# Optimization experiments

Hardware: AMD Instinct MI355X
Metric: run time of the kernel (lower is better)

## Reference

```python
import jax, jax.numpy as jnp
import numpy as np

B, T, S, H, NUM_HEAD = 4, 1024, 1024, 1024, 16
CAUSAL = True
EPS = 1e-5            # torch nn.LayerNorm default
NEG = -float(2 ** 32)  # masked_fill value in the source


def setup_inputs() -> dict:
    key = jax.random.key(0)
    ks = jax.random.split(key, 8)
    queries = jax.random.normal(ks[0], (B, T, H), jnp.float32)
    keys = jax.random.normal(ks[1], (B, S, H), jnp.float32)
    queries_mask = jax.random.randint(ks[2], (B, T, 1), 0, 2).astype(jnp.int32)
    keys_mask = jax.random.randint(ks[3], (B, S, 1), 0, 2).astype(jnp.int32)
    Wq = jax.random.normal(ks[4], (H, H), jnp.float32) * 0.02
    Wk = jax.random.normal(ks[5], (H, H), jnp.float32) * 0.02
    Wv = jax.random.normal(ks[6], (H, H), jnp.float32) * 0.02
    bq = jnp.zeros((H,), jnp.float32)
    bk = jnp.zeros((H,), jnp.float32)
    bv = jnp.zeros((H,), jnp.float32)
    gamma = jnp.ones((H,), jnp.float32)
    beta = jnp.zeros((H,), jnp.float32)
    return {"queries": queries, "queries_mask": queries_mask, "keys": keys,
            "keys_mask": keys_mask, "Wq": Wq, "bq": bq, "Wk": Wk, "bk": bk,
            "Wv": Wv, "bv": bv, "gamma": gamma, "beta": beta}


def _layernorm(x, gamma, beta):
    m = jnp.mean(x, axis=-1, keepdims=True)
    v = jnp.mean((x - m) ** 2, axis=-1, keepdims=True)  # biased var, as torch
    return gamma * (x - m) / jnp.sqrt(v + EPS) + beta


def reference(queries, queries_mask, keys, keys_mask, Wq, bq, Wk, bk, Wv, bv, gamma, beta):
    dh = H // NUM_HEAD
    # ReLU-activated QKV projections (torch Linear: x @ W.T + b)
    Q = jax.nn.relu(queries @ Wq.T + bq)            # (B,T,H)
    K = jax.nn.relu(keys @ Wk.T + bk)               # (B,S,H)
    V = jax.nn.relu(keys @ Wv.T + bv)               # (B,S,H)
    # chunk along feature dim then cat along batch == (h, B, L, dh) layout
    Qh = Q.reshape(B, T, NUM_HEAD, dh).transpose(2, 0, 1, 3)
    Kh = K.reshape(B, S, NUM_HEAD, dh).transpose(2, 0, 1, 3)
    Vh = V.reshape(B, S, NUM_HEAD, dh).transpose(2, 0, 1, 3)
    # scaled by sqrt(hidden_size), NOT sqrt(head_dim) — faithful to source
    scores = jnp.einsum('hbtd,hbsd->hbts', Qh, Kh) / float(np.sqrt(H))
    # padding mask via outer product of the two masks
    qm = queries_mask[..., 0].astype(jnp.float32)   # (B,T)
    km = keys_mask[..., 0].astype(jnp.float32)      # (B,S)
    pad = (qm[:, :, None] * km[:, None, :]) == 0.0  # (B,T,S) True -> masked
    scores = jnp.where(pad[None], NEG, scores)
    if CAUSAL:
        tri = jnp.triu(jnp.ones((T, S), bool), k=1)  # triu(ones)-eye == strict upper
        scores = jnp.where(tri[None, None], NEG, scores)
    attn = jax.nn.softmax(scores, axis=-1)
    out = jnp.einsum('hbts,hbsd->hbtd', attn, Vh)   # (h,B,T,dh)
    out = out.transpose(1, 2, 0, 3).reshape(B, T, H)  # cat heads back on feature dim
    out = out * queries_mask.astype(jnp.float32)
    return _layernorm(out + queries, gamma, beta)
```

## Files before the change

### kernel.cpp

```cpp
#include <hip/hip_runtime.h>
#include <hip/hip_bf16.h>
#include <math.h>

#define B_ 4
#define T_ 1024
#define S_ 1024
#define H_ 1024
#define NH_ 16
#define DH_ 64
#define NEGV -4294967296.0f
#define EPS_ 1e-5f

typedef __attribute__((ext_vector_type(8))) short short8;
typedef __attribute__((ext_vector_type(8))) unsigned short ushort8;
typedef __attribute__((ext_vector_type(4))) unsigned short ushort4v;
typedef __attribute__((ext_vector_type(4))) unsigned int uint4v;
typedef __attribute__((ext_vector_type(4))) float f32x4;

__device__ __forceinline__ unsigned short f2bf(float x) {
    unsigned int u = __float_as_uint(x);
    u += 0x7FFF + ((u >> 16) & 1);
    return (unsigned short)(u >> 16);
}

__device__ __forceinline__ float bf2f(unsigned short u) {
    return __uint_as_float(((unsigned int)u) << 16);
}

__device__ __forceinline__ unsigned int pack_bf16(float a, float b) {
    union { __hip_bfloat162 h; unsigned int u; } cv;
    cv.h = __float22bfloat162_rn(float2{a, b});
    return cv.u;
}

__device__ __forceinline__ void gload16(const unsigned short* g, unsigned short* l) {
    __builtin_amdgcn_global_load_lds(
        (const __attribute__((address_space(1))) unsigned int*)g,
        (__attribute__((address_space(3))) unsigned int*)l,
        16, 0, 0);
}

#define VMCNT(n) asm volatile("s_waitcnt vmcnt(" #n ")" ::: "memory")
#define LGKM0()  { asm volatile("s_waitcnt lgkmcnt(0)" ::: "memory"); \
                   __builtin_amdgcn_sched_barrier(0); }

__global__ __launch_bounds__(256) void cast_bf16(
    const float* __restrict__ q, const float* __restrict__ k,
    const float* __restrict__ wq, const float* __restrict__ wk,
    const float* __restrict__ wv,
    unsigned short* __restrict__ dq, unsigned short* __restrict__ dk,
    unsigned short* __restrict__ dwq, unsigned short* __restrict__ dwk,
    unsigned short* __restrict__ dwv)
{
    const int seg = blockIdx.y;
    const float* src; unsigned short* dst; int n;
    switch (seg) {
        case 0:  src = q;  dst = dq;  n = B_*T_*H_; break;
        case 1:  src = k;  dst = dk;  n = B_*S_*H_; break;
        case 2:  src = wq; dst = dwq; n = H_*H_;    break;
        case 3:  src = wk; dst = dwk; n = H_*H_;    break;
        default: src = wv; dst = dwv; n = H_*H_;    break;
    }
    const int i = (blockIdx.x * 256 + threadIdx.x) * 8;
    if (i >= n) return;
    float4 a = *(const float4*)&src[i];
    float4 b = *(const float4*)&src[i + 4];
    ushort8 o;
    o[0] = f2bf(a.x); o[1] = f2bf(a.y); o[2] = f2bf(a.z); o[3] = f2bf(a.w);
    o[4] = f2bf(b.x); o[5] = f2bf(b.y); o[6] = f2bf(b.z); o[7] = f2bf(b.w);
    *(ushort8*)&dst[i] = o;
}

__global__ __launch_bounds__(512, 4) void qkv_mfma(
    const unsigned short* __restrict__ Xq, const unsigned short* __restrict__ Xk,
    const unsigned short* __restrict__ Wq, const unsigned short* __restrict__ Wk,
    const unsigned short* __restrict__ Wv,
    const float* __restrict__ bq, const float* __restrict__ bk,
    const float* __restrict__ bv,
    unsigned short* __restrict__ Qo, unsigned short* __restrict__ Ko,
    unsigned short* __restrict__ Vo)
{
    const int bi = (blockIdx.x & 7) * 96 + (blockIdx.x >> 3);
    const int col_t = bi >> 5, row_t = bi & 31;
    const int which = col_t >> 3;
    const int colW = (col_t & 7) * 128;
    const int row0 = row_t * 128;

    const unsigned short* X = (which == 0) ? Xq : Xk;
    const unsigned short* Wm = (which == 0) ? Wq : (which == 1) ? Wk : Wv;
    const float* bias        = (which == 0) ? bq : (which == 1) ? bk : bv;
    unsigned short* Out      = (which == 0) ? Qo : (which == 1) ? Ko : Vo;

    __shared__ __align__(16) unsigned short S[32768];

    const int tid = threadIdx.x;
    const int wid = tid >> 6, lane = tid & 63, lo = lane & 15, hi = lane >> 4;
    const int wm = wid >> 2, wn = wid & 3;
    const int swr = (lo & 7) << 3;
    const int csw = ((tid & 7) << 3) ^ (((tid >> 3) & 7) << 3);

    auto stageA = [&](int kt) {
        const int k0 = kt << 6;
        unsigned short* dst = &S[(kt & 1) * 16384 + wid * 512];
        #pragma unroll
        for (int u = 0; u < 2; ++u) {
            const int rowT = row0 + u * 64 + (tid >> 3);
            gload16(&X[(size_t)rowT * H_ + k0 + csw], dst + u * 4096);
        }
    };
    auto stageB = [&](int kt) {
        const int k0 = kt << 6;
        unsigned short* dst = &S[(kt & 1) * 16384 + 8192 + wid * 512];
        #pragma unroll
        for (int u = 0; u < 2; ++u) {
            const int n = u * 64 + (tid >> 3);
            gload16(&Wm[(size_t)(colW + n) * H_ + k0 + csw], dst + u * 4096);
        }
    };

    short8 afr[4][2], bfr[2][2];
    f32x4 acc[4][2] = {};

    auto readA = [&](int boff) {
        #pragma unroll
        for (int i2 = 0; i2 < 4; ++i2)
            #pragma unroll
            for (int kc = 0; kc < 2; ++kc)
                afr[i2][kc] = *(const short8*)
                    &S[boff + (wm*64 + i2*16 + lo)*64 + ((kc*32 + hi*8) ^ swr)];
    };
    auto readB = [&](int boff) {
        #pragma unroll
        for (int j2 = 0; j2 < 2; ++j2)
            #pragma unroll
            for (int kc = 0; kc < 2; ++kc)
                bfr[j2][kc] = *(const short8*)
                    &S[boff + 8192 + (wn*32 + j2*16 + lo)*64 + ((kc*32 + hi*8) ^ swr)];
    };

    float bj[2];
    #pragma unroll
    for (int j2 = 0; j2 < 2; ++j2)
        bj[j2] = bias[colW + wn*32 + j2*16 + lo];

    stageA(0); stageB(0); stageA(1); stageB(1);
    VMCNT(4);
    __builtin_amdgcn_s_barrier();

    for (int it = 0; it < 16; ++it) {
        const int boff = (it & 1) * 16384;
        readA(boff);
        readB(boff);
        LGKM0();
        __builtin_amdgcn_s_barrier();
        if (it <= 13) { stageA(it + 2); stageB(it + 2); }
        __builtin_amdgcn_s_setprio(1);
        #pragma unroll
        for (int i2 = 0; i2 < 4; ++i2)
            #pragma unroll
            for (int j2 = 0; j2 < 2; ++j2)
                #pragma unroll
                for (int kc = 0; kc < 2; ++kc)
                    acc[i2][j2] = __builtin_amdgcn_mfma_f32_16x16x32_bf16(
                        afr[i2][kc], bfr[j2][kc], acc[i2][j2], 0, 0, 0);
        __builtin_amdgcn_s_setprio(0);
        if (it < 14) { VMCNT(4); } else { VMCNT(0); }
        __builtin_amdgcn_s_barrier();
    }

    #pragma unroll
    for (int i2 = 0; i2 < 4; ++i2) {
        const int er = wm*64 + i2*16 + hi*4;
        #pragma unroll
        for (int j2 = 0; j2 < 2; ++j2) {
            const int ec = wn*32 + j2*16 + lo;
            #pragma unroll
            for (int r = 0; r < 4; ++r)
                S[(er + r) * 136 + ec] = f2bf(fmaxf(acc[i2][j2][r] + bj[j2], 0.f));
        }
    }
    __syncthreads();
    #pragma unroll
    for (int u = 0; u < 4; ++u) {
        const int cid = u * 512 + tid;
        const int rr = cid >> 4, ch = cid & 15;
        ushort8 v = *(const ushort8*)&S[rr * 136 + ch * 8];
        *(ushort8*)&Out[(size_t)(row0 + rr) * H_ + colW + ch * 8] = v;
    }
}

__global__ __launch_bounds__(256) void vmean_prep(
    const unsigned short* __restrict__ V, const int* __restrict__ kmask,
    float* __restrict__ vmean_part, int* __restrict__ sfirst)
{
    const int bh = blockIdx.x >> 2, chunk = blockIdx.x & 3;
    const int b = bh >> 4, h = bh & 15;
    const int tid = threadIdx.x;
    const int d8 = tid & 7, sg = tid >> 3;

    __shared__ float red[32][68];
    __shared__ int sf_sh;
    if (tid == 0) sf_sh = S_;

    float acc[8] = {0,0,0,0,0,0,0,0};
    #pragma unroll
    for (int it = 0; it < 8; ++it) {
        const int s = chunk * 256 + sg + it * 32;
        ushort8 v = *(const ushort8*)&V[((size_t)b*S_ + s) * H_ + h*DH_ + d8*8];
        #pragma unroll
        for (int i = 0; i < 8; ++i) acc[i] += bf2f(v[i]);
    }
    #pragma unroll
    for (int i = 0; i < 8; ++i) red[sg][d8*8 + i] = acc[i];

    if (blockIdx.x < B_) {
        int lf = S_;
        #pragma unroll
        for (int u = 0; u < 4; ++u) {
            const int s = tid + u * 256;
            if (kmask[blockIdx.x * S_ + s] != 0) lf = min(lf, s);
        }
        atomicMin(&sf_sh, lf);
    }
    __syncthreads();

    for (int str = 16; str >= 1; str >>= 1) {
        if (sg < str) {
            #pragma unroll
            for (int i = 0; i < 8; ++i)
                red[sg][d8*8 + i] += red[sg + str][d8*8 + i];
        }
        __syncthreads();
    }
    if (tid < 64) vmean_part[blockIdx.x * 64 + tid] = red[0][tid] * (1.f / 1024.f);
    if (blockIdx.x < B_ && tid == 0) sfirst[blockIdx.x] = sf_sh;
}

__global__ __launch_bounds__(256) void attn_mfma(
    const unsigned short* __restrict__ Q, const unsigned short* __restrict__ K,
    const unsigned short* __restrict__ V, const int* __restrict__ kmask,
    const float* __restrict__ vmean_part, const int* __restrict__ sfirst,
    unsigned short* __restrict__ Ob)
{
    const int flat = blockIdx.x;
    const int nf = (flat & 7) * 64 + (flat >> 3);
    const int z = nf & 7, bh = nf >> 3;
    const int b = bh >> 4, h = bh & 15;

    const int tid = threadIdx.x;
    const int wid = tid >> 6, lane = tid & 63, hi = lane >> 4, lo = lane & 15;

    __shared__ unsigned short Ks[2][64][64];
    __shared__ unsigned short Vt[2][64][64];

    const int s_first = sfirst[b];

    const int srow = tid >> 2, d0k = (tid & 3) << 4, swk = (srow & 7) << 3;
    const int sp = tid & 31, dg = tid >> 5;
    const int s2 = sp * 2;
    const int ps = (s2 & 35) | ((s2 & 16) >> 2) | ((s2 & 12) << 1);

    ushort8 krA0, krA1, vrA0, vrA1; int kmA;
    ushort8 krB0, krB1, vrB0, vrB1; int kmB;

    auto stage_load = [&](int s0_, ushort8& k0, ushort8& k1,
                          ushort8& v0, ushort8& v1, int& kmr) {
        const unsigned short* kp = &K[((size_t)b*S_ + s0_ + srow) * H_ + h*DH_ + d0k];
        k0 = *(const ushort8*)kp;
        k1 = *(const ushort8*)(kp + 8);
        const unsigned short* vp = &V[((size_t)b*S_ + s0_ + s2) * H_ + h*DH_ + dg*8];
        v0 = *(const ushort8*)vp;
        v1 = *(const ushort8*)(vp + H_);
        kmr = kmask[b*S_ + s0_ + lane];
    };
    auto stage_write = [&](int pb, const ushort8& k0, const ushort8& k1,
                           const ushort8& v0, const ushort8& v1) {
        *(ushort8*)&Ks[pb][srow][d0k ^ swk]       = k0;
        *(ushort8*)&Ks[pb][srow][(d0k + 8) ^ swk] = k1;
        #pragma unroll
        for (int i = 0; i < 8; ++i) {
            const int d = dg*8 + i;
            const unsigned int pk = (unsigned int)(unsigned short)v0[i]
                                  | ((unsigned int)(unsigned short)v1[i] << 16);
            *(unsigned int*)&Vt[pb][d][ps ^ ((d & 7) << 3)] = pk;
        }
    };

    for (int item = 0; item < 2; ++item) {
        const int qt = item ? z : (15 - z);
        const int t0 = qt * 64;
        const int ntiles = qt + 1;
        const int tq = t0 + wid*16 + lo;

        short8 qf0, qf1;
        {
            const unsigned short* qp =
                &Q[((size_t)b*T_ + t0 + wid*16 + lo) * H_ + h*DH_ + hi*8];
            qf0 = *(const short8*)qp;
            qf1 = *(const short8*)(qp + 32);
        }

        float m = -INFINITY, l = 0.f;
        f32x4 oacc[4] = {{0,0,0,0},{0,0,0,0},{0,0,0,0},{0,0,0,0}};

        auto compute = [&](int pb, int s0, int kmr) {
            const unsigned long long kmb = __ballot(kmr != 0);
            f32x4 sc[4] = {{0,0,0,0},{0,0,0,0},{0,0,0,0},{0,0,0,0}};
            const int swq = (lo & 7) << 3;
            __builtin_amdgcn_s_setprio(1);
            #pragma unroll
            for (int n = 0; n < 4; ++n) {
                short8 kfa = *(const short8*)&Ks[pb][n*16 + lo][(hi*8) ^ swq];
                sc[n] = __builtin_amdgcn_mfma_f32_16x16x32_bf16(kfa, qf0, sc[n], 0, 0, 0);
                short8 kfb = *(const short8*)&Ks[pb][n*16 + lo][(32 + hi*8) ^ swq];
                sc[n] = __builtin_amdgcn_mfma_f32_16x16x32_bf16(kfb, qf1, sc[n], 0, 0, 0);
            }
            __builtin_amdgcn_s_setprio(0);
            float p[4][4];
            float rm = -INFINITY;
            #pragma unroll
            for (int n = 0; n < 4; ++n)
                #pragma unroll
                for (int r = 0; r < 4; ++r) {
                    const int sl = n*16 + hi*4 + r;
                    const bool msk = !((kmb >> sl) & 1ull) || (s0 + sl > tq);
                    const float v = sc[n][r] * 0.03125f;
                    p[n][r] = msk ? NEGV : v;
                    rm = fmaxf(rm, p[n][r]);
                }
            rm = fmaxf(rm, __shfl_xor(rm, 16));
            rm = fmaxf(rm, __shfl_xor(rm, 32));
            if (__any(rm > m + 8.f)) {
                const float mn  = fmaxf(m, rm);
                const float scl = __expf(m - mn);
                m = mn;
                l *= scl;
                #pragma unroll
                for (int r = 0; r < 4; ++r) {
                    const float os = __shfl(scl, hi*4 + r);
                    oacc[0][r] *= os; oacc[1][r] *= os;
                    oacc[2][r] *= os; oacc[3][r] *= os;
                }
            }
            float ts = 0.f;
            #pragma unroll
            for (int n = 0; n < 4; ++n)
                #pragma unroll
                for (int r = 0; r < 4; ++r) {
                    p[n][r] = __expf(p[n][r] - m);
                    ts += p[n][r];
                }
            ts += __shfl_xor(ts, 16);
            ts += __shfl_xor(ts, 32);
            l += ts;
            unsigned int pk0[4], pk1[4];
            #pragma unroll
            for (int n = 0; n < 4; ++n) {
                pk0[n] = pack_bf16(p[n][0], p[n][1]);
                pk1[n] = pack_bf16(p[n][2], p[n][3]);
            }
            __builtin_amdgcn_s_setprio(1);
            #pragma unroll
            for (int cch = 0; cch < 2; ++cch) {
                uint4v u;
                u.x = pk0[2*cch];   u.y = pk1[2*cch];
                u.z = pk0[2*cch+1]; u.w = pk1[2*cch+1];
                const short8 pf = __builtin_bit_cast(short8, u);
                #pragma unroll
                for (int n2 = 0; n2 < 4; ++n2) {
                    const int d = n2*16 + lo;
                    const short8 vf =
                        *(const short8*)&Vt[pb][d][(cch*32 + hi*8) ^ ((d & 7) << 3)];
                    oacc[n2] = __builtin_amdgcn_mfma_f32_16x16x32_bf16(pf, vf, oacc[n2], 0, 0, 0);
                }
            }
            __builtin_amdgcn_s_setprio(0);
        };

        __syncthreads();
        stage_load(0, krA0, krA1, vrA0, vrA1, kmA);
        int t = 0;
        for (;;) {
            stage_write(0, krA0, krA1, vrA0, vrA1);
            if (t + 1 < ntiles) stage_load((t+1) << 6, krB0, krB1, vrB0, vrB1, kmB);
            __syncthreads();
            compute(0, t << 6, kmA);
            if (++t >= ntiles) break;

            stage_write(1, krB0, krB1, vrB0, vrB1);
            if (t + 1 < ntiles) stage_load((t+1) << 6, krA0, krA1, vrA0, vrA1, kmA);
            __syncthreads();
            compute(1, t << 6, kmB);
            if (++t >= ntiles) break;
        }

        const float inv = 1.0f / l;
        #pragma unroll
        for (int r = 0; r < 4; ++r) {
            const float ir = __shfl(inv, hi*4 + r);
            const int trow = t0 + wid*16 + hi*4 + r;
            unsigned short* dst = &Ob[((size_t)b*T_ + trow) * H_ + h*DH_ + lo];
            if (trow < s_first) {
                #pragma unroll
                for (int g = 0; g < 4; ++g) {
                    float vm = vmean_part[(bh*4 + 0)*64 + lo + g*16]
                             + vmean_part[(bh*4 + 1)*64 + lo + g*16]
                             + vmean_part[(bh*4 + 2)*64 + lo + g*16]
                             + vmean_part[(bh*4 + 3)*64 + lo + g*16];
                    dst[g*16] = f2bf(vm);
                }
            } else {
                dst[0]  = f2bf(oacc[0][r] * ir);
                dst[16] = f2bf(oacc[1][r] * ir);
                dst[32] = f2bf(oacc[2][r] * ir);
                dst[48] = f2bf(oacc[3][r] * ir);
            }
        }
    }
}

__global__ __launch_bounds__(256) void ln_kernel(
    const unsigned short* __restrict__ Ob, float* __restrict__ Out,
    const float* __restrict__ queries, const int* __restrict__ qmask,
    const float* __restrict__ gamma, const float* __restrict__ beta)
{
    const int row = blockIdx.x;
    const int tid = threadIdx.x;
    const float qm = (float)qmask[row];

    ushort4v a4 = *(const ushort4v*)&Ob[(size_t)row * H_ + tid*4];
    float4 q4 = *(const float4*)&queries[(size_t)row * H_ + tid*4];
    float x0 = bf2f(a4.x) * qm + q4.x;
    float x1 = bf2f(a4.y) * qm + q4.y;
    float x2 = bf2f(a4.z) * qm + q4.z;
    float x3 = bf2f(a4.w) * qm + q4.w;

    float sum = x0 + x1 + x2 + x3;
    float sq  = x0*x0 + x1*x1 + x2*x2 + x3*x3;
    #pragma unroll
    for (int off = 32; off >= 1; off >>= 1) {
        sum += __shfl_down(sum, off);
        sq  += __shfl_down(sq,  off);
    }
    __shared__ float rs[4], rq[4];
    const int wid = tid >> 6, lane = tid & 63;
    if (lane == 0) { rs[wid] = sum; rq[wid] = sq; }
    __syncthreads();
    const float tot  = rs[0] + rs[1] + rs[2] + rs[3];
    const float totq = rq[0] + rq[1] + rq[2] + rq[3];
    const float mean = tot * (1.f / H_);
    const float var  = totq * (1.f / H_) - mean * mean;
    const float rstd = rsqrtf(var + EPS_);

    float4 g4 = *(const float4*)&gamma[tid*4];
    float4 b4 = *(const float4*)&beta[tid*4];
    float4 y;
    y.x = (x0 - mean) * rstd * g4.x + b4.x;
    y.y = (x1 - mean) * rstd * g4.y + b4.y;
    y.z = (x2 - mean) * rstd * g4.z + b4.z;
    y.w = (x3 - mean) * rstd * g4.w + b4.w;
    *(float4*)&Out[(size_t)row * H_ + tid*4] = y;
}

extern "C" void kernel_launch(void* const* d_in, const int* in_sizes, int n_in,
                              void* d_out, int out_size, void* d_ws, size_t ws_size,
                              hipStream_t stream)
{
    const float* queries = (const float*)d_in[0];
    const int*   qmask   = (const int*)  d_in[1];
    const float* keys    = (const float*)d_in[2];
    const int*   kmask   = (const int*)  d_in[3];
    const float* Wq      = (const float*)d_in[4];
    const float* bq      = (const float*)d_in[5];
    const float* Wk      = (const float*)d_in[6];
    const float* bk      = (const float*)d_in[7];
    const float* Wv      = (const float*)d_in[8];
    const float* bv      = (const float*)d_in[9];
    const float* gamma   = (const float*)d_in[10];
    const float* beta    = (const float*)d_in[11];
    float* out = (float*)d_out;

    unsigned short* Xqb = (unsigned short*)d_ws;
    unsigned short* Xkb = Xqb + (size_t)B_*T_*H_;
    unsigned short* Wqb = Xkb + (size_t)B_*S_*H_;
    unsigned short* Wkb = Wqb + (size_t)H_*H_;
    unsigned short* Wvb = Wkb + (size_t)H_*H_;
    unsigned short* Qb  = Wvb + (size_t)H_*H_;
    unsigned short* Kb  = Qb  + (size_t)B_*T_*H_;
    unsigned short* Vb  = Kb  + (size_t)B_*S_*H_;
    float* vmeanF = (float*)Xqb;
    int*   sfirstI = (int*)(vmeanF + 256*64);
    unsigned short* Ob = Xkb;

    dim3 gc((B_*T_*H_/8 + 255)/256, 5, 1);
    cast_bf16<<<gc, 256, 0, stream>>>(queries, keys, Wq, Wk, Wv,
                                      Xqb, Xkb, Wqb, Wkb, Wvb);

    qkv_mfma<<<768, 512, 0, stream>>>(Xqb, Xkb, Wqb, Wkb, Wvb,
                                      bq, bk, bv, Qb, Kb, Vb);

    vmean_prep<<<256, 256, 0, stream>>>(Vb, kmask, vmeanF, sfirstI);

    attn_mfma<<<512, 256, 0, stream>>>(Qb, Kb, Vb, kmask, vmeanF, sfirstI, Ob);

    ln_kernel<<<B_*T_, 256, 0, stream>>>(Ob, out, queries, qmask, gamma, beta);
}
```

Before: 92.32 us.

## Fuse fp32-to-bf16 activation cast into QKV GEMM A-tile staging

Removes the separate cast pass over queries and keys. The QKV GEMM now loads fp32 activations into registers, converts them to bf16 and writes them to LDS, and a register double buffer keeps the global loads one tile ahead. This saves one write and one read of the bf16 activation copies, but the GEMM reads twice as many activation bytes. It also replaces the async global-to-LDS path for A with register staging, adding VALU conversion work and a full vmcnt(0) wait inside each iteration.

```diff
diff --git a/kernel.cpp b/kernel.cpp
--- a/kernel.cpp
+++ b/kernel.cpp
@@ -45,24 +45,19 @@
                    __builtin_amdgcn_sched_barrier(0); }
 
 __global__ __launch_bounds__(256) void cast_bf16(
-    const float* __restrict__ q, const float* __restrict__ k,
     const float* __restrict__ wq, const float* __restrict__ wk,
     const float* __restrict__ wv,
-    unsigned short* __restrict__ dq, unsigned short* __restrict__ dk,
     unsigned short* __restrict__ dwq, unsigned short* __restrict__ dwk,
     unsigned short* __restrict__ dwv)
 {
     const int seg = blockIdx.y;
-    const float* src; unsigned short* dst; int n;
+    const float* src; unsigned short* dst;
     switch (seg) {
-        case 0:  src = q;  dst = dq;  n = B_*T_*H_; break;
-        case 1:  src = k;  dst = dk;  n = B_*S_*H_; break;
-        case 2:  src = wq; dst = dwq; n = H_*H_;    break;
-        case 3:  src = wk; dst = dwk; n = H_*H_;    break;
-        default: src = wv; dst = dwv; n = H_*H_;    break;
+        case 0:  src = wq; dst = dwq; break;
+        case 1:  src = wk; dst = dwk; break;
+        default: src = wv; dst = dwv; break;
     }
     const int i = (blockIdx.x * 256 + threadIdx.x) * 8;
-    if (i >= n) return;
     float4 a = *(const float4*)&src[i];
     float4 b = *(const float4*)&src[i + 4];
     ushort8 o;
@@ -72,7 +67,7 @@
 }
 
 __global__ __launch_bounds__(512, 4) void qkv_mfma(
-    const unsigned short* __restrict__ Xq, const unsigned short* __restrict__ Xk,
+    const float* __restrict__ Xqf, const float* __restrict__ Xkf,
     const unsigned short* __restrict__ Wq, const unsigned short* __restrict__ Wk,
     const unsigned short* __restrict__ Wv,
     const float* __restrict__ bq, const float* __restrict__ bk,
@@ -86,7 +81,7 @@
     const int colW = (col_t & 7) * 128;
     const int row0 = row_t * 128;
 
-    const unsigned short* X = (which == 0) ? Xq : Xk;
+    const float* Xf = (which == 0) ? Xqf : Xkf;
     const unsigned short* Wm = (which == 0) ? Wq : (which == 1) ? Wk : Wv;
     const float* bias        = (which == 0) ? bq : (which == 1) ? bk : bv;
     unsigned short* Out      = (which == 0) ? Qo : (which == 1) ? Ko : Vo;
@@ -99,13 +94,28 @@
     const int swr = (lo & 7) << 3;
     const int csw = ((tid & 7) << 3) ^ (((tid >> 3) & 7) << 3);
 
-    auto stageA = [&](int kt) {
+    float4 rA[2][4];
+    auto loadA = [&](int kt) {
         const int k0 = kt << 6;
-        unsigned short* dst = &S[(kt & 1) * 16384 + wid * 512];
+        float4* r = rA[kt & 1];
         #pragma unroll
         for (int u = 0; u < 2; ++u) {
             const int rowT = row0 + u * 64 + (tid >> 3);
-            gload16(&X[(size_t)rowT * H_ + k0 + csw], dst + u * 4096);
+            const float* src = &Xf[(size_t)rowT * H_ + k0 + csw];
+            r[u*2]   = *(const float4*)src;
+            r[u*2+1] = *(const float4*)(src + 4);
+        }
+    };
+    auto writeA = [&](int kt) {
+        const float4* r = rA[kt & 1];
+        #pragma unroll
+        for (int u = 0; u < 2; ++u) {
+            ushort8 o;
+            o[0] = f2bf(r[u*2].x);   o[1] = f2bf(r[u*2].y);
+            o[2] = f2bf(r[u*2].z);   o[3] = f2bf(r[u*2].w);
+            o[4] = f2bf(r[u*2+1].x); o[5] = f2bf(r[u*2+1].y);
+            o[6] = f2bf(r[u*2+1].z); o[7] = f2bf(r[u*2+1].w);
+            *(ushort8*)&S[(kt & 1) * 16384 + wid * 512 + u * 4096 + lane * 8] = o;
         }
     };
     auto stageB = [&](int kt) {
@@ -143,8 +153,14 @@
     for (int j2 = 0; j2 < 2; ++j2)
         bj[j2] = bias[colW + wn*32 + j2*16 + lo];
 
-    stageA(0); stageB(0); stageA(1); stageB(1);
+    loadA(0); loadA(1); stageB(0); stageB(1);
+    VMCNT(8);
+    writeA(0);
     VMCNT(4);
+    writeA(1);
+    loadA(2);
+    VMCNT(4);
+    LGKM0();
     __builtin_amdgcn_s_barrier();
 
     for (int it = 0; it < 16; ++it) {
@@ -153,7 +169,14 @@
         readB(boff);
         LGKM0();
         __builtin_amdgcn_s_barrier();
-        if (it <= 13) { stageA(it + 2); stageB(it + 2); }
+        if (it <= 13) {
+            VMCNT(0);
+            writeA(it + 2);
+            stageB(it + 2);
+            if (it <= 12) loadA(it + 3);
+        } else if (it == 14) {
+            VMCNT(0);
+        }
         __builtin_amdgcn_s_setprio(1);
         #pragma unroll
         for (int i2 = 0; i2 < 4; ++i2)
@@ -164,7 +187,6 @@
                     acc[i2][j2] = __builtin_amdgcn_mfma_f32_16x16x32_bf16(
                         afr[i2][kc], bfr[j2][kc], acc[i2][j2], 0, 0, 0);
         __builtin_amdgcn_s_setprio(0);
-        if (it < 14) { VMCNT(4); } else { VMCNT(0); }
         __builtin_amdgcn_s_barrier();
     }
 
@@ -492,11 +514,10 @@
     int*   sfirstI = (int*)(vmeanF + 256*64);
     unsigned short* Ob = Xkb;
 
-    dim3 gc((B_*T_*H_/8 + 255)/256, 5, 1);
-    cast_bf16<<<gc, 256, 0, stream>>>(queries, keys, Wq, Wk, Wv,
-                                      Xqb, Xkb, Wqb, Wkb, Wvb);
-
-    qkv_mfma<<<768, 512, 0, stream>>>(Xqb, Xkb, Wqb, Wkb, Wvb,
+    dim3 gc(H_*H_/8/256, 3, 1);
+    cast_bf16<<<gc, 256, 0, stream>>>(Wq, Wk, Wv, Wqb, Wkb, Wvb);
+
+    qkv_mfma<<<768, 512, 0, stream>>>(queries, keys, Wqb, Wkb, Wvb,
                                       bq, bk, bv, Qb, Kb, Vb);
 
     vmean_prep<<<256, 256, 0, stream>>>(Vb, kmask, vmeanF, sfirstI);
```

New measurement: 218.4 us. 2.37x slower.

## Share K/V tile loads between paired causal query tiles in one pass

Applied to the files above, without the earlier changes.

Instead of processing the high and low query tiles sequentially, each reloading K/V from global memory, the block now streams K/V once and computes both query tiles against each staged tile while the low tile is still within its causal range. This removes the duplicate K/V loads and staging for the low tile and one pass of loop and sync overhead. In exchange it keeps two sets of accumulators and Q fragments live, which raises register pressure and may lower occupancy.

```diff
diff --git a/kernel.cpp b/kernel.cpp
--- a/kernel.cpp
+++ b/kernel.cpp
@@ -286,119 +286,133 @@
         }
     };
 
-    for (int item = 0; item < 2; ++item) {
-        const int qt = item ? z : (15 - z);
-        const int t0 = qt * 64;
-        const int ntiles = qt + 1;
-        const int tq = t0 + wid*16 + lo;
-
-        short8 qf0, qf1;
+    const int qtH = 15 - z, qtL = z;
+    const int t0H = qtH * 64, t0L = qtL * 64;
+    const int ntiles = qtH + 1;
+    const int tqH = t0H + wid*16 + lo;
+    const int tqL = t0L + wid*16 + lo;
+
+    short8 qfH0, qfH1, qfL0, qfL1;
+    {
+        const unsigned short* qp =
+            &Q[((size_t)b*T_ + t0H + wid*16 + lo) * H_ + h*DH_ + hi*8];
+        qfH0 = *(const short8*)qp;
+        qfH1 = *(const short8*)(qp + 32);
+        const unsigned short* qp2 =
+            &Q[((size_t)b*T_ + t0L + wid*16 + lo) * H_ + h*DH_ + hi*8];
+        qfL0 = *(const short8*)qp2;
+        qfL1 = *(const short8*)(qp2 + 32);
+    }
+
+    float mH = -INFINITY, lH = 0.f, mL = -INFINITY, lL = 0.f;
+    f32x4 oH[4] = {{0,0,0,0},{0,0,0,0},{0,0,0,0},{0,0,0,0}};
+    f32x4 oL[4] = {{0,0,0,0},{0,0,0,0},{0,0,0,0},{0,0,0,0}};
+
+    auto compute = [&](int pb, int s0, unsigned long long kmb,
+                       float& m, float& l, f32x4 (&oacc)[4], int tq,
+                       const short8& qf0, const short8& qf1) {
+        f32x4 sc[4] = {{0,0,0,0},{0,0,0,0},{0,0,0,0},{0,0,0,0}};
+        const int swq = (lo & 7) << 3;
+        __builtin_amdgcn_s_setprio(1);
+        #pragma unroll
+        for (int n = 0; n < 4; ++n) {
+            short8 kfa = *(const short8*)&Ks[pb][n*16 + lo][(hi*8) ^ swq];
+            sc[n] = __builtin_amdgcn_mfma_f32_16x16x32_bf16(kfa, qf0, sc[n], 0, 0, 0);
+            short8 kfb = *(const short8*)&Ks[pb][n*16 + lo][(32 + hi*8) ^ swq];
+            sc[n] = __builtin_amdgcn_mfma_f32_16x16x32_bf16(kfb, qf1, sc[n], 0, 0, 0);
+        }
+        __builtin_amdgcn_s_setprio(0);
+        float p[4][4];
+        float rm = -INFINITY;
+        #pragma unroll
+        for (int n = 0; n < 4; ++n)
+            #pragma unroll
+            for (int r = 0; r < 4; ++r) {
+                const int sl = n*16 + hi*4 + r;
+                const bool msk = !((kmb >> sl) & 1ull) || (s0 + sl > tq);
+                const float v = sc[n][r] * 0.03125f;
+                p[n][r] = msk ? NEGV : v;
+                rm = fmaxf(rm, p[n][r]);
+            }
+        rm = fmaxf(rm, __shfl_xor(rm, 16));
+        rm = fmaxf(rm, __shfl_xor(rm, 32));
+        if (__any(rm > m + 8.f)) {
+            const float mn  = fmaxf(m, rm);
+            const float scl = __expf(m - mn);
+            m = mn;
+            l *= scl;
+            #pragma unroll
+            for (int r = 0; r < 4; ++r) {
+                const float os = __shfl(scl, hi*4 + r);
+                oacc[0][r] *= os; oacc[1][r] *= os;
+                oacc[2][r] *= os; oacc[3][r] *= os;
+            }
+        }
+        float ts = 0.f;
+        #pragma unroll
+        for (int n = 0; n < 4; ++n)
+            #pragma unroll
+            for (int r = 0; r < 4; ++r) {
+                p[n][r] = __expf(p[n][r] - m);
+                ts += p[n][r];
+            }
+        ts += __shfl_xor(ts, 16);
+        ts += __shfl_xor(ts, 32);
+        l += ts;
+        unsigned int pk0[4], pk1[4];
+        #pragma unroll
+        for (int n = 0; n < 4; ++n) {
+            pk0[n] = pack_bf16(p[n][0], p[n][1]);
+            pk1[n] = pack_bf16(p[n][2], p[n][3]);
+        }
+        __builtin_amdgcn_s_setprio(1);
+        #pragma unroll
+        for (int cch = 0; cch < 2; ++cch) {
+            uint4v u;
+            u.x = pk0[2*cch];   u.y = pk1[2*cch];
+            u.z = pk0[2*cch+1]; u.w = pk1[2*cch+1];
+            const short8 pf = __builtin_bit_cast(short8, u);
+            #pragma unroll
+            for (int n2 = 0; n2 < 4; ++n2) {
+                const int d = n2*16 + lo;
+                const short8 vf =
+                    *(const short8*)&Vt[pb][d][(cch*32 + hi*8) ^ ((d & 7) << 3)];
+                oacc[n2] = __builtin_amdgcn_mfma_f32_16x16x32_bf16(pf, vf, oacc[n2], 0, 0, 0);
+            }
+        }
+        __builtin_amdgcn_s_setprio(0);
+    };
+
+    stage_load(0, krA0, krA1, vrA0, vrA1, kmA);
+    int t = 0;
+    for (;;) {
+        stage_write(0, krA0, krA1, vrA0, vrA1);
         {
-            const unsigned short* qp =
-                &Q[((size_t)b*T_ + t0 + wid*16 + lo) * H_ + h*DH_ + hi*8];
-            qf0 = *(const short8*)qp;
-            qf1 = *(const short8*)(qp + 32);
-        }
-
-        float m = -INFINITY, l = 0.f;
-        f32x4 oacc[4] = {{0,0,0,0},{0,0,0,0},{0,0,0,0},{0,0,0,0}};
-
-        auto compute = [&](int pb, int s0, int kmr) {
-            const unsigned long long kmb = __ballot(kmr != 0);
-            f32x4 sc[4] = {{0,0,0,0},{0,0,0,0},{0,0,0,0},{0,0,0,0}};
-            const int swq = (lo & 7) << 3;
-            __builtin_amdgcn_s_setprio(1);
-            #pragma unroll
-            for (int n = 0; n < 4; ++n) {
-                short8 kfa = *(const short8*)&Ks[pb][n*16 + lo][(hi*8) ^ swq];
-                sc[n] = __builtin_amdgcn_mfma_f32_16x16x32_bf16(kfa, qf0, sc[n], 0, 0, 0);
-                short8 kfb = *(const short8*)&Ks[pb][n*16 + lo][(32 + hi*8) ^ swq];
-                sc[n] = __builtin_amdgcn_mfma_f32_16x16x32_bf16(kfb, qf1, sc[n], 0, 0, 0);
-            }
-            __builtin_amdgcn_s_setprio(0);
-            float p[4][4];
-            float rm = -INFINITY;
-            #pragma unroll
-            for (int n = 0; n < 4; ++n)
-                #pragma unroll
-                for (int r = 0; r < 4; ++r) {
-                    const int sl = n*16 + hi*4 + r;
-                    const bool msk = !((kmb >> sl) & 1ull) || (s0 + sl > tq);
-                    const float v = sc[n][r] * 0.03125f;
-                    p[n][r] = msk ? NEGV : v;
-                    rm = fmaxf(rm, p[n][r]);
-                }
-            rm = fmaxf(rm, __shfl_xor(rm, 16));
-            rm = fmaxf(rm, __shfl_xor(rm, 32));
-            if (__any(rm > m + 8.f)) {
-                const float mn  = fmaxf(m, rm);
-                const float scl = __expf(m - mn);
-                m = mn;
-                l *= scl;
-                #pragma unroll
-                for (int r = 0; r < 4; ++r) {
-                    const float os = __shfl(scl, hi*4 + r);
-                    oacc[0][r] *= os; oacc[1][r] *= os;
-                    oacc[2][r] *= os; oacc[3][r] *= os;
-                }
-            }
-            float ts = 0.f;
-            #pragma unroll
-            for (int n = 0; n < 4; ++n)
-                #pragma unroll
-                for (int r = 0; r < 4; ++r) {
-                    p[n][r] = __expf(p[n][r] - m);
-                    ts += p[n][r];
-                }
-            ts += __shfl_xor(ts, 16);
-            ts += __shfl_xor(ts, 32);
-            l += ts;
-            unsigned int pk0[4], pk1[4];
-            #pragma unroll
-            for (int n = 0; n < 4; ++n) {
-                pk0[n] = pack_bf16(p[n][0], p[n][1]);
-                pk1[n] = pack_bf16(p[n][2], p[n][3]);
-            }
-            __builtin_amdgcn_s_setprio(1);
-            #pragma unroll
-            for (int cch = 0; cch < 2; ++cch) {
-                uint4v u;
-                u.x = pk0[2*cch];   u.y = pk1[2*cch];
-                u.z = pk0[2*cch+1]; u.w = pk1[2*cch+1];
-                const short8 pf = __builtin_bit_cast(short8, u);
-                #pragma unroll
-                for (int n2 = 0; n2 < 4; ++n2) {
-                    const int d = n2*16 + lo;
-                    const short8 vf =
-                        *(const short8*)&Vt[pb][d][(cch*32 + hi*8) ^ ((d & 7) << 3)];
-                    oacc[n2] = __builtin_amdgcn_mfma_f32_16x16x32_bf16(pf, vf, oacc[n2], 0, 0, 0);
-                }
-            }
-            __builtin_amdgcn_s_setprio(0);
-        };
-
-        __syncthreads();
-        stage_load(0, krA0, krA1, vrA0, vrA1, kmA);
-        int t = 0;
-        for (;;) {
-            stage_write(0, krA0, krA1, vrA0, vrA1);
+            const unsigned long long kb = __ballot(kmA != 0);
             if (t + 1 < ntiles) stage_load((t+1) << 6, krB0, krB1, vrB0, vrB1, kmB);
             __syncthreads();
-            compute(0, t << 6, kmA);
-            if (++t >= ntiles) break;
-
-            stage_write(1, krB0, krB1, vrB0, vrB1);
+            compute(0, t << 6, kb, mH, lH, oH, tqH, qfH0, qfH1);
+            if (t <= qtL) compute(0, t << 6, kb, mL, lL, oL, tqL, qfL0, qfL1);
+        }
+        if (++t >= ntiles) break;
+
+        stage_write(1, krB0, krB1, vrB0, vrB1);
+        {
+            const unsigned long long kb = __ballot(kmB != 0);
             if (t + 1 < ntiles) stage_load((t+1) << 6, krA0, krA1, vrA0, vrA1, kmA);
             __syncthreads();
-            compute(1, t << 6, kmB);
-            if (++t >= ntiles) break;
-        }
-
-        const float inv = 1.0f / l;
+            compute(1, t << 6, kb, mH, lH, oH, tqH, qfH0, qfH1);
+            if (t <= qtL) compute(1, t << 6, kb, mL, lL, oL, tqL, qfL0, qfL1);
+        }
+        if (++t >= ntiles) break;
+    }
+
+    {
+        const float inv = 1.0f / lH;
         #pragma unroll
         for (int r = 0; r < 4; ++r) {
             const float ir = __shfl(inv, hi*4 + r);
-            const int trow = t0 + wid*16 + hi*4 + r;
+            const int trow = t0H + wid*16 + hi*4 + r;
             unsigned short* dst = &Ob[((size_t)b*T_ + trow) * H_ + h*DH_ + lo];
             if (trow < s_first) {
                 #pragma unroll
@@ -410,10 +424,34 @@
                     dst[g*16] = f2bf(vm);
                 }
             } else {
-                dst[0]  = f2bf(oacc[0][r] * ir);
-                dst[16] = f2bf(oacc[1][r] * ir);
-                dst[32] = f2bf(oacc[2][r] * ir);
-                dst[48] = f2bf(oacc[3][r] * ir);
+                dst[0]  = f2bf(oH[0][r] * ir);
+                dst[16] = f2bf(oH[1][r] * ir);
+                dst[32] = f2bf(oH[2][r] * ir);
+                dst[48] = f2bf(oH[3][r] * ir);
+            }
+        }
+    }
+    {
+        const float inv = 1.0f / lL;
+        #pragma unroll
+        for (int r = 0; r < 4; ++r) {
+            const float ir = __shfl(inv, hi*4 + r);
+            const int trow = t0L + wid*16 + hi*4 + r;
+            unsigned short* dst = &Ob[((size_t)b*T_ + trow) * H_ + h*DH_ + lo];
+            if (trow < s_first) {
+                #pragma unroll
+                for (int g = 0; g < 4; ++g) {
+                    float vm = vmean_part[(bh*4 + 0)*64 + lo + g*16]
+                             + vmean_part[(bh*4 + 1)*64 + lo + g*16]
+                             + vmean_part[(bh*4 + 2)*64 + lo + g*16]
+                             + vmean_part[(bh*4 + 3)*64 + lo + g*16];
+                    dst[g*16] = f2bf(vm);
+                }
+            } else {
+                dst[0]  = f2bf(oL[0][r] * ir);
+                dst[16] = f2bf(oL[1][r] * ir);
+                dst[32] = f2bf(oL[2][r] * ir);
+                dst[48] = f2bf(oL[3][r] * ir);
             }
         }
     }
```

Result: slower. 104.2 us (+12.9%).
